# Kernel tuning notes

Measured on AMD Instinct MI355X. Metric: run time of the kernel, lower is better.

Reference implementation:

```python
import jax, jax.numpy as jnp
import numpy as np

OUT_H = 7  # _height_
OUT_W = 7  # _width_


def _bin_ids(start, end, size, nbins):
    # Per-pixel segment id along one spatial axis; id == nbins marks pixels outside the ROI.
    # Mirrors TF: step = int(region / nbins); bin i covers [i*step, (i+1)*step), last bin extends to region end.
    step = ((end - start).astype(jnp.float32) / nbins).astype(jnp.int32)
    idx = jnp.arange(size)
    rel = idx - start
    b = jnp.minimum(rel // jnp.maximum(step, 1), nbins - 1)
    b = jnp.where(step > 0, b, nbins - 1)  # degenerate step==0: everything valid falls in last bin
    valid = (rel >= 0) & (idx < end)
    return jnp.where(valid, b, nbins)


def _pool_one(fmap, roi):
    # fmap: [H, W, C], roi: [4] = (h_min, w_min, h_max, w_max) relative coords
    H, W, C = fmap.shape
    h0 = (H * roi[0]).astype(jnp.int32)
    w0 = (W * roi[1]).astype(jnp.int32)
    h1 = (H * roi[2]).astype(jnp.int32)
    w1 = (W * roi[3]).astype(jnp.int32)
    colb = _bin_ids(w0, w1, W, OUT_W)  # [W]
    rowb = _bin_ids(h0, h1, H, OUT_H)  # [H]
    # Max is separable over rows/cols: pool columns first, then rows.
    tmp = jax.ops.segment_max(jnp.transpose(fmap, (1, 0, 2)), colb, num_segments=OUT_W + 1)[:OUT_W]  # [OUT_W, H, C]
    out = jax.ops.segment_max(jnp.transpose(tmp, (1, 0, 2)), rowb, num_segments=OUT_H + 1)[:OUT_H]   # [OUT_H, OUT_W, C]
    return out


def _roi_pool(feature_map, rois):
    per_image = jax.vmap(_pool_one, in_axes=(None, 0))  # over ROIs
    return jax.vmap(per_image)(feature_map, rois)       # over batch -> [B, R, OUT_H, OUT_W, C]


def setup_inputs() -> dict:
    key = jax.random.key(0)
    k1, k2, k3 = jax.random.split(key, 3)
    B, H, W, C, R = 4, 56, 56, 256, 64
    feature_map = jax.random.normal(k1, (B, H, W, C), dtype=jnp.float32)
    # valid ROIs: (h_min, w_min) in [0, 0.45), extent in [0.30, 0.55) so every 7x7 bin is non-empty
    starts = jax.random.uniform(k2, (B, R, 2), minval=0.0, maxval=0.45, dtype=jnp.float32)
    lens = jax.random.uniform(k3, (B, R, 2), minval=0.30, maxval=0.55, dtype=jnp.float32)
    rois = jnp.concatenate([starts, jnp.minimum(starts + lens, 1.0)], axis=-1)  # [B, R, 4]
    return {"feature_map": feature_map, "rois": rois}


def reference(feature_map, rois):
    return _roi_pool(feature_map, rois)
```

## Files before the change

kernel.cpp:

```cpp
#include <hip/hip_runtime.h>


#define OUT_H 7
#define OUT_W 7
#define NBIN (OUT_H * OUT_W)
#define NB 4
#define NR 64
#define NH 56
#define NW 56
#define NC 256
#define C4 (NC / 4)

#define BLKS_PER_XCD_SLOT 1568

typedef float v4f __attribute__((ext_vector_type(4)));

__device__ __forceinline__ v4f vmax4(v4f a, v4f b) {
    v4f r;
    r.x = fmaxf(a.x, b.x);
    r.y = fmaxf(a.y, b.y);
    r.z = fmaxf(a.z, b.z);
    r.w = fmaxf(a.w, b.w);
    return r;
}

__global__ __launch_bounds__(256) void roi_pool_kernel(
    const float* __restrict__ fmap,
    const float* __restrict__ rois,
    float* __restrict__ out)
{
    __shared__ v4f red[3][64];

    const int blk  = blockIdx.x;
    const int xcd  = blk & 7;
    const int b    = xcd >> 1;
    const int wid  = threadIdx.x >> 6;
    const int lane = threadIdx.x & 63;

    const int work = ((xcd & 1) * BLKS_PER_XCD_SLOT) + (blk >> 3);
    const int r    = work / NBIN;
    const int bin  = work - r * NBIN;
    const int oi   = bin / OUT_W;
    const int oj   = bin - oi * OUT_W;

    const float* roi = rois + (size_t)(b * NR + r) * 4;
    const float r0 = roi[0], r1 = roi[1], r2 = roi[2], r3 = roi[3];
    const int h0 = (int)((float)NH * r0);
    const int w0 = (int)((float)NW * r1);
    const int h1 = (int)((float)NH * r2);
    const int w1 = (int)((float)NW * r3);

    const int hstep = (int)((float)(h1 - h0) / (float)OUT_H);
    const int wstep = (int)((float)(w1 - w0) / (float)OUT_W);

    int rlo, rhi, clo, chi;
    if (hstep >= 1) {
        rlo = h0 + oi * hstep;
        rhi = (oi < OUT_H - 1) ? (rlo + hstep) : h1;
    } else {
        rlo = (oi == OUT_H - 1) ? h0 : 0;
        rhi = (oi == OUT_H - 1) ? h1 : 0;
    }
    if (wstep >= 1) {
        clo = w0 + oj * wstep;
        chi = (oj < OUT_W - 1) ? (clo + wstep) : w1;
    } else {
        clo = (oj == OUT_W - 1) ? w0 : 0;
        chi = (oj == OUT_W - 1) ? w1 : 0;
    }

    const v4f* base =
        (const v4f*)(fmap + (size_t)b * NH * NW * NC) + lane;

    const v4f ninf = (v4f){-INFINITY, -INFINITY, -INFINITY, -INFINITY};
    v4f acc0 = ninf, acc1 = ninf, acc2 = ninf, acc3 = ninf;

    const int wstart = clo + wid;

    int h = rlo;
    for (; h + 1 < rhi; h += 2) {
        const v4f* r0p = base + (size_t)(h * NW) * C4;
        const v4f* r1p = r0p + (size_t)NW * C4;
        int w = wstart;
        for (; w + 4 < chi; w += 8) {
            acc0 = vmax4(acc0, r0p[(size_t)w * C4]);
            acc1 = vmax4(acc1, r0p[(size_t)(w + 4) * C4]);
            acc2 = vmax4(acc2, r1p[(size_t)w * C4]);
            acc3 = vmax4(acc3, r1p[(size_t)(w + 4) * C4]);
        }
        if (w < chi) {
            acc0 = vmax4(acc0, r0p[(size_t)w * C4]);
            acc2 = vmax4(acc2, r1p[(size_t)w * C4]);
        }
    }
    if (h < rhi) {
        const v4f* r0p = base + (size_t)(h * NW) * C4;
        int w = wstart;
        for (; w + 4 < chi; w += 8) {
            acc0 = vmax4(acc0, r0p[(size_t)w * C4]);
            acc1 = vmax4(acc1, r0p[(size_t)(w + 4) * C4]);
        }
        if (w < chi) acc0 = vmax4(acc0, r0p[(size_t)w * C4]);
    }

    v4f acc = vmax4(vmax4(acc0, acc1), vmax4(acc2, acc3));

    if (wid > 0) red[wid - 1][lane] = acc;
    __syncthreads();

    if (wid == 0) {
        acc = vmax4(acc, red[0][lane]);
        acc = vmax4(acc, vmax4(red[1][lane], red[2][lane]));
        const size_t obase = ((size_t)((b * NR + r) * NBIN + bin)) * NC;
        v4f* o = (v4f*)(out + obase);
        __builtin_nontemporal_store(acc, o + lane);
    }
}

extern "C" void kernel_launch(void* const* d_in, const int* in_sizes, int n_in,
                              void* d_out, int out_size, void* d_ws, size_t ws_size,
                              hipStream_t stream) {
    const float* fmap = (const float*)d_in[0];
    const float* rois = (const float*)d_in[1];
    float* out = (float*)d_out;

    const int nblocks = NB * NR * NBIN;
    roi_pool_kernel<<<nblocks, 256, 0, stream>>>(fmap, rois, out);
}
```

Baseline: 18.44 us.

## Assign whole bins to single wavefronts, two bins each, with permuted bin order

Instead of four wavefronts splitting each output bin's columns and reducing through shared memory, each wavefront now pools an entire bin on its own and handles two bins. A multiplicative permutation spreads bins across wavefronts for load balance, and the grid shrinks eightfold. This removes the LDS reduction and __syncthreads and cuts block-launch overhead. In exchange each wavefront's serial work grows and occupancy depends on the launch-bound hint.

```diff
diff --git a/kernel.cpp b/kernel.cpp
--- a/kernel.cpp
+++ b/kernel.cpp
@@ -11,7 +11,10 @@
 #define NC 256
 #define C4 (NC / 4)
 
-#define BLKS_PER_XCD_SLOT 1568
+#define NBLOCKS 1568
+#define BLKS_PER_XCD_SLOT 196
+#define BINS_PER_IMG (NR * NBIN)
+#define PERM_MUL 597
 
 typedef float v4f __attribute__((ext_vector_type(4)));
 
@@ -24,69 +27,22 @@
     return r;
 }
 
-__global__ __launch_bounds__(256) void roi_pool_kernel(
-    const float* __restrict__ fmap,
-    const float* __restrict__ rois,
-    float* __restrict__ out)
+__device__ __forceinline__ v4f pool_window(
+    const v4f* __restrict__ base, int rlo, int rhi, int clo, int chi)
 {
-    __shared__ v4f red[3][64];
-
-    const int blk  = blockIdx.x;
-    const int xcd  = blk & 7;
-    const int b    = xcd >> 1;
-    const int wid  = threadIdx.x >> 6;
-    const int lane = threadIdx.x & 63;
-
-    const int work = ((xcd & 1) * BLKS_PER_XCD_SLOT) + (blk >> 3);
-    const int r    = work / NBIN;
-    const int bin  = work - r * NBIN;
-    const int oi   = bin / OUT_W;
-    const int oj   = bin - oi * OUT_W;
-
-    const float* roi = rois + (size_t)(b * NR + r) * 4;
-    const float r0 = roi[0], r1 = roi[1], r2 = roi[2], r3 = roi[3];
-    const int h0 = (int)((float)NH * r0);
-    const int w0 = (int)((float)NW * r1);
-    const int h1 = (int)((float)NH * r2);
-    const int w1 = (int)((float)NW * r3);
-
-    const int hstep = (int)((float)(h1 - h0) / (float)OUT_H);
-    const int wstep = (int)((float)(w1 - w0) / (float)OUT_W);
-
-    int rlo, rhi, clo, chi;
-    if (hstep >= 1) {
-        rlo = h0 + oi * hstep;
-        rhi = (oi < OUT_H - 1) ? (rlo + hstep) : h1;
-    } else {
-        rlo = (oi == OUT_H - 1) ? h0 : 0;
-        rhi = (oi == OUT_H - 1) ? h1 : 0;
-    }
-    if (wstep >= 1) {
-        clo = w0 + oj * wstep;
-        chi = (oj < OUT_W - 1) ? (clo + wstep) : w1;
-    } else {
-        clo = (oj == OUT_W - 1) ? w0 : 0;
-        chi = (oj == OUT_W - 1) ? w1 : 0;
-    }
-
-    const v4f* base =
-        (const v4f*)(fmap + (size_t)b * NH * NW * NC) + lane;
-
     const v4f ninf = (v4f){-INFINITY, -INFINITY, -INFINITY, -INFINITY};
     v4f acc0 = ninf, acc1 = ninf, acc2 = ninf, acc3 = ninf;
-
-    const int wstart = clo + wid;
 
     int h = rlo;
     for (; h + 1 < rhi; h += 2) {
         const v4f* r0p = base + (size_t)(h * NW) * C4;
         const v4f* r1p = r0p + (size_t)NW * C4;
-        int w = wstart;
-        for (; w + 4 < chi; w += 8) {
+        int w = clo;
+        for (; w + 1 < chi; w += 2) {
             acc0 = vmax4(acc0, r0p[(size_t)w * C4]);
-            acc1 = vmax4(acc1, r0p[(size_t)(w + 4) * C4]);
+            acc1 = vmax4(acc1, r0p[(size_t)(w + 1) * C4]);
             acc2 = vmax4(acc2, r1p[(size_t)w * C4]);
-            acc3 = vmax4(acc3, r1p[(size_t)(w + 4) * C4]);
+            acc3 = vmax4(acc3, r1p[(size_t)(w + 1) * C4]);
         }
         if (w < chi) {
             acc0 = vmax4(acc0, r0p[(size_t)w * C4]);
@@ -95,25 +51,74 @@
     }
     if (h < rhi) {
         const v4f* r0p = base + (size_t)(h * NW) * C4;
-        int w = wstart;
-        for (; w + 4 < chi; w += 8) {
+        int w = clo;
+        for (; w + 1 < chi; w += 2) {
             acc0 = vmax4(acc0, r0p[(size_t)w * C4]);
-            acc1 = vmax4(acc1, r0p[(size_t)(w + 4) * C4]);
+            acc1 = vmax4(acc1, r0p[(size_t)(w + 1) * C4]);
         }
         if (w < chi) acc0 = vmax4(acc0, r0p[(size_t)w * C4]);
     }
+    return vmax4(vmax4(acc0, acc1), vmax4(acc2, acc3));
+}
 
-    v4f acc = vmax4(vmax4(acc0, acc1), vmax4(acc2, acc3));
+__global__ __launch_bounds__(256, 8) void roi_pool_kernel(
+    const float* __restrict__ fmap,
+    const float* __restrict__ rois,
+    float* __restrict__ out)
+{
+    const int blk  = blockIdx.x;
+    const int xcd  = blk & 7;
+    const int b    = xcd >> 1;
+    const int wid  = threadIdx.x >> 6;
+    const int lane = threadIdx.x & 63;
 
-    if (wid > 0) red[wid - 1][lane] = acc;
-    __syncthreads();
+    const int ibl = ((xcd & 1) * BLKS_PER_XCD_SLOT) + (blk >> 3);
+    const int iw  = ibl * 4 + wid;
 
-    if (wid == 0) {
-        acc = vmax4(acc, red[0][lane]);
-        acc = vmax4(acc, vmax4(red[1][lane], red[2][lane]));
+    const v4f* base =
+        (const v4f*)(fmap + (size_t)b * NH * NW * NC) + lane;
+    const float* roib = rois + (size_t)b * NR * 4;
+
+#pragma unroll
+    for (int t = 0; t < 2; ++t) {
+        const int j    = 2 * iw + t;
+        const int gbin = (j * PERM_MUL) % BINS_PER_IMG;
+        const int r    = gbin / NBIN;
+        const int bin  = gbin - r * NBIN;
+        const int oi   = bin / OUT_W;
+        const int oj   = bin - oi * OUT_W;
+
+        const float* roi = roib + (size_t)r * 4;
+        const float r0 = roi[0], r1 = roi[1], r2 = roi[2], r3 = roi[3];
+        const int h0 = (int)((float)NH * r0);
+        const int w0 = (int)((float)NW * r1);
+        const int h1 = (int)((float)NH * r2);
+        const int w1 = (int)((float)NW * r3);
+
+        const int hstep = (int)((float)(h1 - h0) / (float)OUT_H);
+        const int wstep = (int)((float)(w1 - w0) / (float)OUT_W);
+
+        int rlo, rhi, clo, chi;
+        if (hstep >= 1) {
+            rlo = h0 + oi * hstep;
+            rhi = (oi < OUT_H - 1) ? (rlo + hstep) : h1;
+        } else {
+            rlo = (oi == OUT_H - 1) ? h0 : 0;
+            rhi = (oi == OUT_H - 1) ? h1 : 0;
+        }
+        if (wstep >= 1) {
+            clo = w0 + oj * wstep;
+            chi = (oj < OUT_W - 1) ? (clo + wstep) : w1;
+        } else {
+            clo = (oj == OUT_W - 1) ? w0 : 0;
+            chi = (oj == OUT_W - 1) ? w1 : 0;
+        }
+
+        const v4f m = pool_window(base, rlo, rhi, clo, chi);
+
         const size_t obase = ((size_t)((b * NR + r) * NBIN + bin)) * NC;
         v4f* o = (v4f*)(out + obase);
-        __builtin_nontemporal_store(acc, o + lane);
+        __builtin_nontemporal_store(m, o + lane);
     }
 }
 
@@ -124,6 +129,5 @@
     const float* rois = (const float*)d_in[1];
     float* out = (float*)d_out;
 
-    const int nblocks = NB * NR * NBIN;
-    roi_pool_kernel<<<nblocks, 256, 0, stream>>>(fmap, rois, out);
+    roi_pool_kernel<<<NBLOCKS, 256, 0, stream>>>(fmap, rois, out);
 }
```

New measurement: 16.27 us. -11.8%, faster.
